# Performance work log

Hardware: AMD Instinct MI355X
Metric: run time of the kernel (lower is better)

Reference implementation:

```python
import jax, jax.numpy as jnp
import numpy as np

NUM_EXPERTS = 8
TOP_K = 2
D = 2048   # hidden_dim
F = 4096   # ffn_dim


def setup_inputs() -> dict:
    key = jax.random.key(0)
    k0, k1, k2, k3, k4 = jax.random.split(key, 5)
    hidden_states = jax.random.normal(k0, (2, 2048, D), dtype=jnp.float32)
    gate_w = jax.random.normal(k1, (NUM_EXPERTS, D), dtype=jnp.float32) * 0.02
    w1 = jax.random.normal(k2, (NUM_EXPERTS, F, D), dtype=jnp.float32) * 0.02
    w2 = jax.random.normal(k3, (NUM_EXPERTS, D, F), dtype=jnp.float32) * 0.02
    w3 = jax.random.normal(k4, (NUM_EXPERTS, F, D), dtype=jnp.float32) * 0.02
    return {"hidden_states": hidden_states, "gate_w": gate_w, "w1": w1, "w2": w2, "w3": w3}


def reference(hidden_states, gate_w, w1, w2, w3):
    B, S, Dm = hidden_states.shape
    h = hidden_states.reshape(-1, Dm)                      # [T, D]
    router_logits = h @ gate_w.T                           # [T, E]
    rw = jax.nn.softmax(router_logits.astype(jnp.float32), axis=-1)
    rw, selected = jax.lax.top_k(rw, TOP_K)                # [T, K], [T, K]
    rw = rw / jnp.sum(rw, axis=-1, keepdims=True)
    rw = rw.astype(h.dtype)
    final = jnp.zeros_like(h)
    for e in range(NUM_EXPERTS):                            # small fixed loop over experts
        w = jnp.sum(rw * (selected == e), axis=1, keepdims=True)  # [T, 1]
        gated = jax.nn.silu(h @ w1[e].T) * (h @ w3[e].T)   # [T, F]
        final = final + (gated @ w2[e].T) * w              # [T, D]
    return final.reshape(B, S, Dm), router_logits
```

## Files before the change

kernel.cpp:

```cpp
#include <hip/hip_runtime.h>
#include <hip/hip_bf16.h>
#include <stdint.h>

#define NE 8
#define TKK 2
#define DD 2048
#define FF 4096
#define TT 4096

typedef __attribute__((ext_vector_type(8))) short bf16x8;
typedef __attribute__((ext_vector_type(4))) float f32x4;

__device__ inline unsigned short f2bf(float f) {
  union { float f; unsigned u; } x; x.f = f;
  unsigned r = x.u + 0x7fffu + ((x.u >> 16) & 1u);
  return (unsigned short)(r >> 16);
}

__device__ inline bf16x8 cvt8(float4 a, float4 b) {
  union { unsigned short h[8]; bf16x8 v; } x;
  x.h[0] = f2bf(a.x); x.h[1] = f2bf(a.y); x.h[2] = f2bf(a.z); x.h[3] = f2bf(a.w);
  x.h[4] = f2bf(b.x); x.h[5] = f2bf(b.y); x.h[6] = f2bf(b.z); x.h[7] = f2bf(b.w);
  return x.v;
}

#define GLL16(g, l) __builtin_amdgcn_global_load_lds( \
    (__attribute__((address_space(1))) void*)(void*)(g), \
    (__attribute__((address_space(3))) void*)(l), 16, 0, 0)

__global__ void convert_kernel(const float* __restrict__ src, unsigned short* __restrict__ dst, long n) {
  long i = ((long)blockIdx.x * 256 + threadIdx.x) * 8;
  long stride = (long)gridDim.x * 256 * 8;
  for (; i < n; i += stride) {
    float4 a = *(const float4*)(src + i);
    float4 b = *(const float4*)(src + i + 4);
    union { unsigned short h[8]; uint4 v; } o;
    o.h[0] = f2bf(a.x); o.h[1] = f2bf(a.y); o.h[2] = f2bf(a.z); o.h[3] = f2bf(a.w);
    o.h[4] = f2bf(b.x); o.h[5] = f2bf(b.y); o.h[6] = f2bf(b.z); o.h[7] = f2bf(b.w);
    *(uint4*)(dst + i) = o.v;
  }
}

__global__ void router_kernel(const float* __restrict__ h, const float* __restrict__ gw,
                              float* __restrict__ logits, unsigned short* __restrict__ hb,
                              int* __restrict__ counts, int* __restrict__ tok_idx,
                              int* __restrict__ sel_e, int* __restrict__ sel_slot,
                              float* __restrict__ sel_w) {
  int t = blockIdx.x;
  int lane = threadIdx.x;
  const float4* hr = (const float4*)(h + (size_t)t * DD);
  float4 hv[8];
  float acc[NE];
#pragma unroll
  for (int e = 0; e < NE; e++) acc[e] = 0.f;
#pragma unroll
  for (int j = 0; j < 8; j++) hv[j] = hr[j * 64 + lane];
  ushort4* hbr = (ushort4*)(hb + (size_t)t * DD);
#pragma unroll
  for (int j = 0; j < 8; j++) {
    ushort4 o;
    o.x = f2bf(hv[j].x); o.y = f2bf(hv[j].y); o.z = f2bf(hv[j].z); o.w = f2bf(hv[j].w);
    hbr[j * 64 + lane] = o;
  }
#pragma unroll
  for (int e = 0; e < NE; e++) {
    const float4* g = (const float4*)(gw + (size_t)e * DD);
    float a = 0.f;
#pragma unroll
    for (int j = 0; j < 8; j++) {
      float4 gv = g[j * 64 + lane];
      a += hv[j].x * gv.x + hv[j].y * gv.y + hv[j].z * gv.z + hv[j].w * gv.w;
    }
    acc[e] = a;
  }
#pragma unroll
  for (int e = 0; e < NE; e++) {
    float v = acc[e];
#pragma unroll
    for (int o = 32; o > 0; o >>= 1) v += __shfl_xor(v, o, 64);
    acc[e] = v;
  }
  if (lane == 0) {
#pragma unroll
    for (int e = 0; e < NE; e++) logits[(size_t)t * NE + e] = acc[e];
    int e1 = 0; float m1 = acc[0];
#pragma unroll
    for (int e = 1; e < NE; e++) if (acc[e] > m1) { m1 = acc[e]; e1 = e; }
    int e2 = -1; float m2 = -3.4e38f;
#pragma unroll
    for (int e = 0; e < NE; e++) if (e != e1 && acc[e] > m2) { m2 = acc[e]; e2 = e; }
    float s = expf(m2 - m1);
    float wa = 1.f / (1.f + s);
    float wb = s * wa;
    int s1 = atomicAdd(&counts[e1], 1);
    tok_idx[e1 * TT + s1] = t;
    int s2 = atomicAdd(&counts[e2], 1);
    tok_idx[e2 * TT + s2] = t;
    sel_e[2 * t] = e1; sel_slot[2 * t] = s1; sel_w[2 * t] = wa;
    sel_e[2 * t + 1] = e2; sel_slot[2 * t + 1] = s2; sel_w[2 * t + 1] = wb;
  }
}

__global__ void offsets_kernel(const int* __restrict__ counts, int* __restrict__ offsets) {
  if (threadIdx.x == 0) {
    int r = 0;
    for (int e = 0; e < NE; e++) { offsets[e] = r; r += counts[e]; }
  }
}

template <bool WB16>
__global__ __launch_bounds__(256) void gemm1_kernel(
    const float* __restrict__ w1f, const float* __restrict__ w3f,
    const unsigned short* __restrict__ w1b, const unsigned short* __restrict__ w3b,
    const unsigned short* __restrict__ hb, const int* __restrict__ tok_idx,
    const int* __restrict__ counts, const int* __restrict__ offsets,
    unsigned short* __restrict__ gated) {
  __shared__ __align__(16) char lds[WB16 ? 32768 : 49152];
  char* Ab = lds;
  char* B1 = lds + 16384;
  char* B3 = lds + (WB16 ? 24576 : 32768);

  int bid = blockIdx.x;
  int x = bid & 7;
  int rest = bid >> 3;
  int m = rest & 31;
  int q = rest >> 5;
  int p = x + 8 * q;
  int n = p & 63;
  int e = p >> 6;
  int cnt = counts[e];
  int row0 = m * 128;
  if (row0 >= cnt) return;
  int offe = offsets[e];
  int tid = threadIdx.x;

  long asrc[4];
#pragma unroll
  for (int i = 0; i < 4; i++) {
    int r = i * 32 + (tid >> 3);
    int rr = row0 + r; if (rr >= cnt) rr = cnt - 1;
    int tok = tok_idx[e * TT + rr];
    asrc[i] = (long)tok * DD + (((tid & 7) ^ (r & 7)) * 8);
  }
  int fbase = n * 64;
  long ebase = (long)e * FF * DD;
  long bsrc[4];
  if constexpr (WB16) {
#pragma unroll
    for (int i = 0; i < 2; i++) {
      int r = i * 32 + (tid >> 3);
      bsrc[i] = ebase + (long)(fbase + r) * DD + (((tid & 7) ^ (r & 7)) * 8);
    }
  } else {
#pragma unroll
    for (int i = 0; i < 4; i++) {
      int r = i * 16 + (tid >> 4);
      bsrc[i] = ebase + (long)(fbase + r) * DD + (((tid & 15) ^ (r & 15)) * 4);
    }
  }

  f32x4 acc1[4][2], acc3[4][2];
#pragma unroll
  for (int i = 0; i < 4; i++)
#pragma unroll
    for (int j = 0; j < 2; j++) { acc1[i][j] = (f32x4){0,0,0,0}; acc3[i][j] = (f32x4){0,0,0,0}; }

  int wv = tid >> 6;
  int lane = tid & 63;
  int wr = (wv >> 1) * 64;
  int wc = (wv & 1) * 32;
  int lrow = lane & 15;
  int lk4 = lane >> 4;

  for (int k0 = 0; k0 < DD; k0 += 64) {
    if (k0) __syncthreads();
#pragma unroll
    for (int i = 0; i < 4; i++)
      GLL16(hb + asrc[i] + k0, Ab + i * 4096 + tid * 16);
    if constexpr (WB16) {
#pragma unroll
      for (int i = 0; i < 2; i++) {
        GLL16(w1b + bsrc[i] + k0, B1 + i * 4096 + tid * 16);
        GLL16(w3b + bsrc[i] + k0, B3 + i * 4096 + tid * 16);
      }
    } else {
#pragma unroll
      for (int i = 0; i < 4; i++) {
        GLL16(w1f + bsrc[i] + k0, B1 + i * 4096 + tid * 16);
        GLL16(w3f + bsrc[i] + k0, B3 + i * 4096 + tid * 16);
      }
    }
    __syncthreads();
#pragma unroll
    for (int kk = 0; kk < 2; kk++) {
      int kseg = kk * 4 + lk4;
      int fs = kk * 8 + lk4 * 2;
      bf16x8 af[4], b1f[2], b3f[2];
#pragma unroll
      for (int i = 0; i < 4; i++) {
        int row = wr + i * 16 + lrow;
        af[i] = *(const bf16x8*)(Ab + row * 128 + ((kseg ^ (row & 7)) * 16));
      }
#pragma unroll
      for (int j = 0; j < 2; j++) {
        int row = wc + j * 16 + lrow;
        if constexpr (WB16) {
          int off = row * 128 + ((kseg ^ (row & 7)) * 16);
          b1f[j] = *(const bf16x8*)(B1 + off);
          b3f[j] = *(const bf16x8*)(B3 + off);
        } else {
          int rx = row & 15;
          float4 a0 = *(const float4*)(B1 + row * 256 + ((fs ^ rx) * 16));
          float4 a1 = *(const float4*)(B1 + row * 256 + (((fs + 1) ^ rx) * 16));
          b1f[j] = cvt8(a0, a1);
          float4 c0 = *(const float4*)(B3 + row * 256 + ((fs ^ rx) * 16));
          float4 c1 = *(const float4*)(B3 + row * 256 + (((fs + 1) ^ rx) * 16));
          b3f[j] = cvt8(c0, c1);
        }
      }
#pragma unroll
      for (int i = 0; i < 4; i++)
#pragma unroll
        for (int j = 0; j < 2; j++) {
          acc1[i][j] = __builtin_amdgcn_mfma_f32_16x16x32_bf16(af[i], b1f[j], acc1[i][j], 0, 0, 0);
          acc3[i][j] = __builtin_amdgcn_mfma_f32_16x16x32_bf16(af[i], b3f[j], acc3[i][j], 0, 0, 0);
        }
    }
  }
  int crow0 = wr + (lane >> 4) * 4;
  int ccol0 = wc + (lane & 15);
#pragma unroll
  for (int i = 0; i < 4; i++)
#pragma unroll
    for (int j = 0; j < 2; j++)
#pragma unroll
      for (int r = 0; r < 4; r++) {
        int trow = crow0 + i * 16 + r;
        if (row0 + trow < cnt) {
          float g = acc1[i][j][r];
          float sg = g / (1.f + __expf(-g));
          float val = sg * acc3[i][j][r];
          gated[(size_t)(offe + row0 + trow) * FF + (fbase + ccol0 + j * 16)] = f2bf(val);
        }
      }
}

template <bool WB16>
__global__ __launch_bounds__(256) void gemm2_kernel(
    const float* __restrict__ w2f, const unsigned short* __restrict__ w2b,
    const unsigned short* __restrict__ gated,
    const int* __restrict__ counts, const int* __restrict__ offsets,
    float* __restrict__ eout) {
  __shared__ __align__(16) char lds[WB16 ? 32768 : 49152];
  char* Ab = lds;
  char* Bb = lds + 16384;

  int bid = blockIdx.x;
  int x = bid & 7;
  int rest = bid >> 3;
  int m = rest & 31;
  int q = rest >> 5;
  int p = x + 8 * q;
  int n = p & 15;
  int e = p >> 4;
  int cnt = counts[e];
  int row0 = m * 128;
  if (row0 >= cnt) return;
  int offe = offsets[e];
  int tid = threadIdx.x;

  long asrc[4];
#pragma unroll
  for (int i = 0; i < 4; i++) {
    int r = i * 32 + (tid >> 3);
    int rr = row0 + r; if (rr >= cnt) rr = cnt - 1;
    asrc[i] = (long)(offe + rr) * FF + (((tid & 7) ^ (r & 7)) * 8);
  }
  int dbase = n * 128;
  long ebase = (long)e * DD * FF;
  long bsrc[8];
  if constexpr (WB16) {
#pragma unroll
    for (int i = 0; i < 4; i++) {
      int r = i * 32 + (tid >> 3);
      bsrc[i] = ebase + (long)(dbase + r) * FF + (((tid & 7) ^ (r & 7)) * 8);
    }
  } else {
#pragma unroll
    for (int i = 0; i < 8; i++) {
      int r = i * 16 + (tid >> 4);
      bsrc[i] = ebase + (long)(dbase + r) * FF + (((tid & 15) ^ (r & 15)) * 4);
    }
  }

  f32x4 acc[4][4];
#pragma unroll
  for (int i = 0; i < 4; i++)
#pragma unroll
    for (int j = 0; j < 4; j++) acc[i][j] = (f32x4){0,0,0,0};

  int wv = tid >> 6;
  int lane = tid & 63;
  int wr = (wv >> 1) * 64;
  int wc = (wv & 1) * 64;
  int lrow = lane & 15;
  int lk4 = lane >> 4;

  for (int k0 = 0; k0 < FF; k0 += 64) {
    if (k0) __syncthreads();
#pragma unroll
    for (int i = 0; i < 4; i++)
      GLL16(gated + asrc[i] + k0, Ab + i * 4096 + tid * 16);
    if constexpr (WB16) {
#pragma unroll
      for (int i = 0; i < 4; i++)
        GLL16(w2b + bsrc[i] + k0, Bb + i * 4096 + tid * 16);
    } else {
#pragma unroll
      for (int i = 0; i < 8; i++)
        GLL16(w2f + bsrc[i] + k0, Bb + i * 4096 + tid * 16);
    }
    __syncthreads();
#pragma unroll
    for (int kk = 0; kk < 2; kk++) {
      int kseg = kk * 4 + lk4;
      int fs = kk * 8 + lk4 * 2;
      bf16x8 af[4], bf[4];
#pragma unroll
      for (int i = 0; i < 4; i++) {
        int row = wr + i * 16 + lrow;
        af[i] = *(const bf16x8*)(Ab + row * 128 + ((kseg ^ (row & 7)) * 16));
      }
#pragma unroll
      for (int j = 0; j < 4; j++) {
        int row = wc + j * 16 + lrow;
        if constexpr (WB16) {
          bf[j] = *(const bf16x8*)(Bb + row * 128 + ((kseg ^ (row & 7)) * 16));
        } else {
          int rx = row & 15;
          float4 a0 = *(const float4*)(Bb + row * 256 + ((fs ^ rx) * 16));
          float4 a1 = *(const float4*)(Bb + row * 256 + (((fs + 1) ^ rx) * 16));
          bf[j] = cvt8(a0, a1);
        }
      }
#pragma unroll
      for (int i = 0; i < 4; i++)
#pragma unroll
        for (int j = 0; j < 4; j++)
          acc[i][j] = __builtin_amdgcn_mfma_f32_16x16x32_bf16(af[i], bf[j], acc[i][j], 0, 0, 0);
    }
  }
  int crow0 = wr + (lane >> 4) * 4;
  int ccol0 = wc + (lane & 15);
#pragma unroll
  for (int i = 0; i < 4; i++)
#pragma unroll
    for (int j = 0; j < 4; j++)
#pragma unroll
      for (int r = 0; r < 4; r++) {
        int trow = crow0 + i * 16 + r;
        if (row0 + trow < cnt)
          eout[(size_t)(offe + row0 + trow) * DD + (dbase + ccol0 + j * 16)] = acc[i][j][r];
      }
}

__global__ void gather_kernel(const float* __restrict__ eout, const int* __restrict__ offsets,
                              const int* __restrict__ sel_e, const int* __restrict__ sel_slot,
                              const float* __restrict__ sel_w, float* __restrict__ out) {
  int idx = blockIdx.x * 256 + threadIdx.x;
  int t = idx >> 9;
  int c = idx & 511;
  int ea = sel_e[2 * t], eb = sel_e[2 * t + 1];
  int sa = offsets[ea] + sel_slot[2 * t];
  int sb = offsets[eb] + sel_slot[2 * t + 1];
  float wa = sel_w[2 * t], wb = sel_w[2 * t + 1];
  float4 va = ((const float4*)(eout + (size_t)sa * DD))[c];
  float4 vb = ((const float4*)(eout + (size_t)sb * DD))[c];
  float4 o;
  o.x = wa * va.x + wb * vb.x;
  o.y = wa * va.y + wb * vb.y;
  o.z = wa * va.z + wb * vb.z;
  o.w = wa * va.w + wb * vb.w;
  ((float4*)(out + (size_t)t * DD))[c] = o;
}

extern "C" void kernel_launch(void* const* d_in, const int* in_sizes, int n_in,
                              void* d_out, int out_size, void* d_ws, size_t ws_size,
                              hipStream_t stream) {
  const float* h  = (const float*)d_in[0];
  const float* gw = (const float*)d_in[1];
  const float* w1 = (const float*)d_in[2];
  const float* w2 = (const float*)d_in[3];
  const float* w3 = (const float*)d_in[4];
  float* out = (float*)d_out;
  float* logits = out + (size_t)TT * DD;

  char* wp = (char*)d_ws;
  int* counts = (int*)wp; wp += 256;
  int* offsets = (int*)wp; wp += 256;
  int* tok_idx = (int*)wp; wp += (size_t)NE * TT * 4;
  int* sel_e = (int*)wp; wp += (size_t)TT * 2 * 4;
  int* sel_slot = (int*)wp; wp += (size_t)TT * 2 * 4;
  float* sel_w = (float*)wp; wp += (size_t)TT * 2 * 4;
  unsigned short* hb = (unsigned short*)wp; wp += (size_t)TT * DD * 2;
  unsigned short* gated = (unsigned short*)wp; wp += (size_t)TT * TKK * FF * 2;
  float* eout = (float*)wp; wp += (size_t)TT * TKK * DD * 4;
  if ((size_t)(wp - (char*)d_ws) > ws_size) return;

  long nw = (long)NE * FF * DD;
  unsigned short* w1b = (unsigned short*)wp; wp += (size_t)nw * 2;
  unsigned short* w3b = (unsigned short*)wp; wp += (size_t)nw * 2;
  unsigned short* w2b = (unsigned short*)wp; wp += (size_t)nw * 2;
  bool wb16 = ((size_t)(wp - (char*)d_ws) <= ws_size);

  hipMemsetAsync(counts, 0, 32, stream);
  router_kernel<<<TT, 64, 0, stream>>>(h, gw, logits, hb, counts, tok_idx, sel_e, sel_slot, sel_w);
  offsets_kernel<<<1, 64, 0, stream>>>(counts, offsets);
  if (wb16) {
    convert_kernel<<<4096, 256, 0, stream>>>(w1, w1b, nw);
    convert_kernel<<<4096, 256, 0, stream>>>(w3, w3b, nw);
    convert_kernel<<<4096, 256, 0, stream>>>(w2, w2b, nw);
    gemm1_kernel<true><<<8 * 32 * 64, 256, 0, stream>>>(w1, w3, w1b, w3b, hb, tok_idx, counts, offsets, gated);
    gemm2_kernel<true><<<8 * 32 * 16, 256, 0, stream>>>(w2, w2b, gated, counts, offsets, eout);
  } else {
    gemm1_kernel<false><<<8 * 32 * 64, 256, 0, stream>>>(w1, w3, nullptr, nullptr, hb, tok_idx, counts, offsets, gated);
    gemm2_kernel<false><<<8 * 32 * 16, 256, 0, stream>>>(w2, nullptr, gated, counts, offsets, eout);
  }
  gather_kernel<<<(TT * DD / 4) / 256, 256, 0, stream>>>(eout, offsets, sel_e, sel_slot, sel_w, out);
}
```

Baseline: 860.6 us.

## Fuse weight conversion into router and gemm1 launches to overlap stages

Merges the w1/w3 fp32-to-bf16 conversion with the router into one prep kernel, with router blocks handling four tokens each. The w2 conversion moves into extra leading blocks of the gemm1 launch. This cuts separate launches and lets conversion bandwidth work overlap with router and gemm1 compute. The cost is fewer conversion blocks per launch, and the gemm1 tiles may be scheduled behind the w2 conversion blocks.

```diff
diff --git a/kernel.cpp b/kernel.cpp
--- a/kernel.cpp
+++ b/kernel.cpp
@@ -7,6 +7,8 @@
 #define DD 2048
 #define FF 4096
 #define TT 4096
+#define CONV13 2048
+#define CONV2  1024
 
 typedef __attribute__((ext_vector_type(8))) short bf16x8;
 typedef __attribute__((ext_vector_type(4))) float f32x4;
@@ -24,30 +26,25 @@
   return x.v;
 }
 
+__device__ __forceinline__ void conv8(const float* __restrict__ src,
+                                      unsigned short* __restrict__ dst, long i) {
+  float4 a = *(const float4*)(src + i);
+  float4 b = *(const float4*)(src + i + 4);
+  union { unsigned short h[8]; uint4 v; } o;
+  o.h[0] = f2bf(a.x); o.h[1] = f2bf(a.y); o.h[2] = f2bf(a.z); o.h[3] = f2bf(a.w);
+  o.h[4] = f2bf(b.x); o.h[5] = f2bf(b.y); o.h[6] = f2bf(b.z); o.h[7] = f2bf(b.w);
+  *(uint4*)(dst + i) = o.v;
+}
+
 #define GLL16(g, l) __builtin_amdgcn_global_load_lds( \
     (__attribute__((address_space(1))) void*)(void*)(g), \
     (__attribute__((address_space(3))) void*)(l), 16, 0, 0)
 
-__global__ void convert_kernel(const float* __restrict__ src, unsigned short* __restrict__ dst, long n) {
-  long i = ((long)blockIdx.x * 256 + threadIdx.x) * 8;
-  long stride = (long)gridDim.x * 256 * 8;
-  for (; i < n; i += stride) {
-    float4 a = *(const float4*)(src + i);
-    float4 b = *(const float4*)(src + i + 4);
-    union { unsigned short h[8]; uint4 v; } o;
-    o.h[0] = f2bf(a.x); o.h[1] = f2bf(a.y); o.h[2] = f2bf(a.z); o.h[3] = f2bf(a.w);
-    o.h[4] = f2bf(b.x); o.h[5] = f2bf(b.y); o.h[6] = f2bf(b.z); o.h[7] = f2bf(b.w);
-    *(uint4*)(dst + i) = o.v;
-  }
-}
-
-__global__ void router_kernel(const float* __restrict__ h, const float* __restrict__ gw,
-                              float* __restrict__ logits, unsigned short* __restrict__ hb,
-                              int* __restrict__ counts, int* __restrict__ tok_idx,
-                              int* __restrict__ sel_e, int* __restrict__ sel_slot,
-                              float* __restrict__ sel_w) {
-  int t = blockIdx.x;
-  int lane = threadIdx.x;
+__device__ __forceinline__ void router_one(
+    int t, int lane, const float* __restrict__ h, const float* __restrict__ gw,
+    float* __restrict__ logits, unsigned short* __restrict__ hb,
+    int* __restrict__ counts, int* __restrict__ tok_idx,
+    int* __restrict__ sel_e, int* __restrict__ sel_slot, float* __restrict__ sel_w) {
   const float4* hr = (const float4*)(h + (size_t)t * DD);
   float4 hv[8];
   float acc[NE];
@@ -101,6 +98,36 @@
   }
 }
 
+__global__ void router_kernel(const float* __restrict__ h, const float* __restrict__ gw,
+                              float* __restrict__ logits, unsigned short* __restrict__ hb,
+                              int* __restrict__ counts, int* __restrict__ tok_idx,
+                              int* __restrict__ sel_e, int* __restrict__ sel_slot,
+                              float* __restrict__ sel_w) {
+  router_one(blockIdx.x, threadIdx.x, h, gw, logits, hb, counts, tok_idx, sel_e, sel_slot, sel_w);
+}
+
+__global__ __launch_bounds__(256) void prep_kernel(
+    const float* __restrict__ h, const float* __restrict__ gw,
+    float* __restrict__ logits, unsigned short* __restrict__ hb,
+    int* __restrict__ counts, int* __restrict__ tok_idx,
+    int* __restrict__ sel_e, int* __restrict__ sel_slot, float* __restrict__ sel_w,
+    const float* __restrict__ w1, unsigned short* __restrict__ w1b,
+    const float* __restrict__ w3, unsigned short* __restrict__ w3b) {
+  if (blockIdx.x < CONV13) {
+    long nw = (long)NE * FF * DD;
+    long i = ((long)blockIdx.x * 256 + threadIdx.x) * 8;
+    long stride = (long)CONV13 * 256 * 8;
+    for (; i < 2 * nw; i += stride) {
+      if (i < nw) conv8(w1, w1b, i);
+      else        conv8(w3, w3b, i - nw);
+    }
+    return;
+  }
+  int b = blockIdx.x - CONV13;
+  router_one(b * 4 + (threadIdx.x >> 6), threadIdx.x & 63,
+             h, gw, logits, hb, counts, tok_idx, sel_e, sel_slot, sel_w);
+}
+
 __global__ void offsets_kernel(const int* __restrict__ counts, int* __restrict__ offsets) {
   if (threadIdx.x == 0) {
     int r = 0;
@@ -108,17 +135,132 @@
   }
 }
 
-template <bool WB16>
-__global__ __launch_bounds__(256) void gemm1_kernel(
-    const float* __restrict__ w1f, const float* __restrict__ w3f,
+__global__ __launch_bounds__(256) void gemm1c_kernel(
     const unsigned short* __restrict__ w1b, const unsigned short* __restrict__ w3b,
     const unsigned short* __restrict__ hb, const int* __restrict__ tok_idx,
     const int* __restrict__ counts, const int* __restrict__ offsets,
-    unsigned short* __restrict__ gated) {
-  __shared__ __align__(16) char lds[WB16 ? 32768 : 49152];
+    unsigned short* __restrict__ gated,
+    const float* __restrict__ w2f, unsigned short* __restrict__ w2b) {
+  __shared__ __align__(16) char lds[32768];
   char* Ab = lds;
   char* B1 = lds + 16384;
-  char* B3 = lds + (WB16 ? 24576 : 32768);
+  char* B3 = lds + 24576;
+
+  if (blockIdx.x < CONV2) {
+    long nw = (long)NE * FF * DD;
+    long i = ((long)blockIdx.x * 256 + threadIdx.x) * 8;
+    long stride = (long)CONV2 * 256 * 8;
+    for (; i < nw; i += stride) conv8(w2f, w2b, i);
+    return;
+  }
+
+  int bid = blockIdx.x - CONV2;
+  int x = bid & 7;
+  int rest = bid >> 3;
+  int m = rest & 31;
+  int q = rest >> 5;
+  int p = x + 8 * q;
+  int n = p & 63;
+  int e = p >> 6;
+  int cnt = counts[e];
+  int row0 = m * 128;
+  if (row0 >= cnt) return;
+  int offe = offsets[e];
+  int tid = threadIdx.x;
+
+  long asrc[4];
+#pragma unroll
+  for (int i = 0; i < 4; i++) {
+    int r = i * 32 + (tid >> 3);
+    int rr = row0 + r; if (rr >= cnt) rr = cnt - 1;
+    int tok = tok_idx[e * TT + rr];
+    asrc[i] = (long)tok * DD + (((tid & 7) ^ (r & 7)) * 8);
+  }
+  int fbase = n * 64;
+  long ebase = (long)e * FF * DD;
+  long bsrc[2];
+#pragma unroll
+  for (int i = 0; i < 2; i++) {
+    int r = i * 32 + (tid >> 3);
+    bsrc[i] = ebase + (long)(fbase + r) * DD + (((tid & 7) ^ (r & 7)) * 8);
+  }
+
+  f32x4 acc1[4][2], acc3[4][2];
+#pragma unroll
+  for (int i = 0; i < 4; i++)
+#pragma unroll
+    for (int j = 0; j < 2; j++) { acc1[i][j] = (f32x4){0,0,0,0}; acc3[i][j] = (f32x4){0,0,0,0}; }
+
+  int wv = tid >> 6;
+  int lane = tid & 63;
+  int wr = (wv >> 1) * 64;
+  int wc = (wv & 1) * 32;
+  int lrow = lane & 15;
+  int lk4 = lane >> 4;
+
+  for (int k0 = 0; k0 < DD; k0 += 64) {
+    if (k0) __syncthreads();
+#pragma unroll
+    for (int i = 0; i < 4; i++)
+      GLL16(hb + asrc[i] + k0, Ab + i * 4096 + tid * 16);
+#pragma unroll
+    for (int i = 0; i < 2; i++) {
+      GLL16(w1b + bsrc[i] + k0, B1 + i * 4096 + tid * 16);
+      GLL16(w3b + bsrc[i] + k0, B3 + i * 4096 + tid * 16);
+    }
+    __syncthreads();
+#pragma unroll
+    for (int kk = 0; kk < 2; kk++) {
+      int kseg = kk * 4 + lk4;
+      bf16x8 af[4], b1f[2], b3f[2];
+#pragma unroll
+      for (int i = 0; i < 4; i++) {
+        int row = wr + i * 16 + lrow;
+        af[i] = *(const bf16x8*)(Ab + row * 128 + ((kseg ^ (row & 7)) * 16));
+      }
+#pragma unroll
+      for (int j = 0; j < 2; j++) {
+        int row = wc + j * 16 + lrow;
+        int off = row * 128 + ((kseg ^ (row & 7)) * 16);
+        b1f[j] = *(const bf16x8*)(B1 + off);
+        b3f[j] = *(const bf16x8*)(B3 + off);
+      }
+#pragma unroll
+      for (int i = 0; i < 4; i++)
+#pragma unroll
+        for (int j = 0; j < 2; j++) {
+          acc1[i][j] = __builtin_amdgcn_mfma_f32_16x16x32_bf16(af[i], b1f[j], acc1[i][j], 0, 0, 0);
+          acc3[i][j] = __builtin_amdgcn_mfma_f32_16x16x32_bf16(af[i], b3f[j], acc3[i][j], 0, 0, 0);
+        }
+    }
+  }
+  int crow0 = wr + (lane >> 4) * 4;
+  int ccol0 = wc + (lane & 15);
+#pragma unroll
+  for (int i = 0; i < 4; i++)
+#pragma unroll
+    for (int j = 0; j < 2; j++)
+#pragma unroll
+      for (int r = 0; r < 4; r++) {
+        int trow = crow0 + i * 16 + r;
+        if (row0 + trow < cnt) {
+          float g = acc1[i][j][r];
+          float sg = g / (1.f + __expf(-g));
+          float val = sg * acc3[i][j][r];
+          gated[(size_t)(offe + row0 + trow) * FF + (fbase + ccol0 + j * 16)] = f2bf(val);
+        }
+      }
+}
+
+__global__ __launch_bounds__(256) void gemm1_kernel_fb(
+    const float* __restrict__ w1f, const float* __restrict__ w3f,
+    const unsigned short* __restrict__ hb, const int* __restrict__ tok_idx,
+    const int* __restrict__ counts, const int* __restrict__ offsets,
+    unsigned short* __restrict__ gated) {
+  __shared__ __align__(16) char lds[49152];
+  char* Ab = lds;
+  char* B1 = lds + 16384;
+  char* B3 = lds + 32768;
 
   int bid = blockIdx.x;
   int x = bid & 7;
@@ -145,18 +287,10 @@
   int fbase = n * 64;
   long ebase = (long)e * FF * DD;
   long bsrc[4];
-  if constexpr (WB16) {
-#pragma unroll
-    for (int i = 0; i < 2; i++) {
-      int r = i * 32 + (tid >> 3);
-      bsrc[i] = ebase + (long)(fbase + r) * DD + (((tid & 7) ^ (r & 7)) * 8);
-    }
-  } else {
-#pragma unroll
-    for (int i = 0; i < 4; i++) {
-      int r = i * 16 + (tid >> 4);
-      bsrc[i] = ebase + (long)(fbase + r) * DD + (((tid & 15) ^ (r & 15)) * 4);
-    }
+#pragma unroll
+  for (int i = 0; i < 4; i++) {
+    int r = i * 16 + (tid >> 4);
+    bsrc[i] = ebase + (long)(fbase + r) * DD + (((tid & 15) ^ (r & 15)) * 4);
   }
 
   f32x4 acc1[4][2], acc3[4][2];
@@ -177,18 +311,10 @@
 #pragma unroll
     for (int i = 0; i < 4; i++)
       GLL16(hb + asrc[i] + k0, Ab + i * 4096 + tid * 16);
-    if constexpr (WB16) {
-#pragma unroll
-      for (int i = 0; i < 2; i++) {
-        GLL16(w1b + bsrc[i] + k0, B1 + i * 4096 + tid * 16);
-        GLL16(w3b + bsrc[i] + k0, B3 + i * 4096 + tid * 16);
-      }
-    } else {
-#pragma unroll
-      for (int i = 0; i < 4; i++) {
-        GLL16(w1f + bsrc[i] + k0, B1 + i * 4096 + tid * 16);
-        GLL16(w3f + bsrc[i] + k0, B3 + i * 4096 + tid * 16);
-      }
+#pragma unroll
+    for (int i = 0; i < 4; i++) {
+      GLL16(w1f + bsrc[i] + k0, B1 + i * 4096 + tid * 16);
+      GLL16(w3f + bsrc[i] + k0, B3 + i * 4096 + tid * 16);
     }
     __syncthreads();
 #pragma unroll
@@ -204,19 +330,13 @@
 #pragma unroll
       for (int j = 0; j < 2; j++) {
         int row = wc + j * 16 + lrow;
-        if constexpr (WB16) {
-          int off = row * 128 + ((kseg ^ (row & 7)) * 16);
-          b1f[j] = *(const bf16x8*)(B1 + off);
-          b3f[j] = *(const bf16x8*)(B3 + off);
-        } else {
-          int rx = row & 15;
-          float4 a0 = *(const float4*)(B1 + row * 256 + ((fs ^ rx) * 16));
-          float4 a1 = *(const float4*)(B1 + row * 256 + (((fs + 1) ^ rx) * 16));
-          b1f[j] = cvt8(a0, a1);
-          float4 c0 = *(const float4*)(B3 + row * 256 + ((fs ^ rx) * 16));
-          float4 c1 = *(const float4*)(B3 + row * 256 + (((fs + 1) ^ rx) * 16));
-          b3f[j] = cvt8(c0, c1);
-        }
+        int rx = row & 15;
+        float4 a0 = *(const float4*)(B1 + row * 256 + ((fs ^ rx) * 16));
+        float4 a1 = *(const float4*)(B1 + row * 256 + (((fs + 1) ^ rx) * 16));
+        b1f[j] = cvt8(a0, a1);
+        float4 c0 = *(const float4*)(B3 + row * 256 + ((fs ^ rx) * 16));
+        float4 c1 = *(const float4*)(B3 + row * 256 + (((fs + 1) ^ rx) * 16));
+        b3f[j] = cvt8(c0, c1);
       }
 #pragma unroll
       for (int i = 0; i < 4; i++)
@@ -414,16 +534,17 @@
   bool wb16 = ((size_t)(wp - (char*)d_ws) <= ws_size);
 
   hipMemsetAsync(counts, 0, 32, stream);
-  router_kernel<<<TT, 64, 0, stream>>>(h, gw, logits, hb, counts, tok_idx, sel_e, sel_slot, sel_w);
-  offsets_kernel<<<1, 64, 0, stream>>>(counts, offsets);
   if (wb16) {
-    convert_kernel<<<4096, 256, 0, stream>>>(w1, w1b, nw);
-    convert_kernel<<<4096, 256, 0, stream>>>(w3, w3b, nw);
-    convert_kernel<<<4096, 256, 0, stream>>>(w2, w2b, nw);
-    gemm1_kernel<true><<<8 * 32 * 64, 256, 0, stream>>>(w1, w3, w1b, w3b, hb, tok_idx, counts, offsets, gated);
+    prep_kernel<<<CONV13 + TT / 4, 256, 0, stream>>>(
+        h, gw, logits, hb, counts, tok_idx, sel_e, sel_slot, sel_w, w1, w1b, w3, w3b);
+    offsets_kernel<<<1, 64, 0, stream>>>(counts, offsets);
+    gemm1c_kernel<<<CONV2 + 8 * 32 * 64, 256, 0, stream>>>(
+        w1b, w3b, hb, tok_idx, counts, offsets, gated, w2, w2b);
     gemm2_kernel<true><<<8 * 32 * 16, 256, 0, stream>>>(w2, w2b, gated, counts, offsets, eout);
   } else {
-    gemm1_kernel<false><<<8 * 32 * 64, 256, 0, stream>>>(w1, w3, nullptr, nullptr, hb, tok_idx, counts, offsets, gated);
+    router_kernel<<<TT, 64, 0, stream>>>(h, gw, logits, hb, counts, tok_idx, sel_e, sel_slot, sel_w);
+    offsets_kernel<<<1, 64, 0, stream>>>(counts, offsets);
+    gemm1_kernel_fb<<<8 * 32 * 64, 256, 0, stream>>>(w1, w3, hb, tok_idx, counts, offsets, gated);
     gemm2_kernel<false><<<8 * 32 * 16, 256, 0, stream>>>(w2, nullptr, gated, counts, offsets, eout);
   }
   gather_kernel<<<(TT * DD / 4) / 256, 256, 0, stream>>>(eout, offsets, sel_e, sel_slot, sel_w, out);
```

Measured after the change: 850.0 us. Within noise of the previous version (-1.2%).
